# Kernel tuning notes

Measured on AMD Instinct MI355X. Metric: run time of the kernel, lower is better.

The kernel has to match this reference:

```python
import jax, jax.numpy as jnp
import numpy as np

K = 3        # deform kernel size
PAD = 1      # autopad(3)
STRIDE = 1

def _conv2d(x, w, b, stride, pad):
    out = jax.lax.conv_general_dilated(
        x, w, (stride, stride), [(pad, pad), (pad, pad)],
        dimension_numbers=('NCHW', 'OIHW', 'NCHW'))
    return out + b[None, :, None, None]

def setup_inputs() -> dict:
    key = jax.random.key(0)
    k1, k2, k3 = jax.random.split(key, 3)
    B, C1, C2, H, W = 16, 128, 128, 80, 80
    x = jax.random.normal(k1, (B, C1, H, W), dtype=jnp.float32)
    # offset-predicting conv: 2*K*K output channels, 3x3 kernel
    offset_w = jax.random.normal(k2, (2 * K * K, C1, 3, 3), dtype=jnp.float32) * 0.05
    offset_b = jnp.zeros((2 * K * K,), dtype=jnp.float32)
    fan_in = C1 * K * K
    weight = jax.random.normal(k3, (C2, C1, K, K), dtype=jnp.float32) * (1.0 / np.sqrt(fan_in))
    bias = jnp.zeros((C2,), dtype=jnp.float32)
    return {'x': x, 'offset_w': offset_w, 'offset_b': offset_b,
            'weight': weight, 'bias': bias}

def _deform_conv(x, offset, weight, bias):
    # x: [B,C,H,W]; offset: [B,2*K*K,Ho,Wo] in (dy,dx) pairs per kernel tap
    B, C, H, W = x.shape
    c2 = weight.shape[0]
    Ho, Wo = offset.shape[2], offset.shape[3]
    off = offset.reshape(B, K * K, 2, Ho, Wo)
    dy, dx = off[:, :, 0], off[:, :, 1]             # [B,KK,Ho,Wo]
    ii, jj = jnp.meshgrid(jnp.arange(K), jnp.arange(K), indexing='ij')
    ki = ii.reshape(-1).astype(jnp.float32)          # [KK]
    kj = jj.reshape(-1).astype(jnp.float32)
    hg = (jnp.arange(Ho) * STRIDE - PAD).astype(jnp.float32)
    wg = (jnp.arange(Wo) * STRIDE - PAD).astype(jnp.float32)
    py = hg[None, None, :, None] + ki[None, :, None, None] + dy  # [B,KK,Ho,Wo]
    px = wg[None, None, None, :] + kj[None, :, None, None] + dx
    y0 = jnp.floor(py); x0 = jnp.floor(px)
    wy1 = py - y0; wy0 = 1.0 - wy1
    wx1 = px - x0; wx0 = 1.0 - wx1

    def corner(yc, xc, wgt):
        valid = (yc >= 0) & (yc < H) & (xc >= 0) & (xc < W)
        yi = jnp.clip(yc, 0, H - 1).astype(jnp.int32)
        xi = jnp.clip(xc, 0, W - 1).astype(jnp.int32)
        # gather per batch: [B,C,KK,Ho,Wo]
        v = jax.vmap(lambda xb, yb, xb2: xb[:, yb, xb2])(x, yi, xi)
        return v * (wgt * valid.astype(x.dtype))[:, None]

    sampled = (corner(y0, x0, wy0 * wx0) + corner(y0, x0 + 1, wy0 * wx1)
               + corner(y0 + 1, x0, wy1 * wx0) + corner(y0 + 1, x0 + 1, wy1 * wx1))
    # grouped weighted sum (g=1): weight [c2, C, K, K] -> [c2, C, KK]
    out = jnp.einsum('bcphw,ocp->bohw', sampled, weight.reshape(c2, C, K * K))
    return out + bias[None, :, None, None]

def reference(x, offset_w, offset_b, weight, bias):
    offset = _conv2d(x, offset_w, offset_b, STRIDE, 1)  # [B, 2*K*K, Ho, Wo]
    return _deform_conv(x, offset, weight, bias)
```

## Files before the change

kernel.cpp:

```cpp
#include <hip/hip_runtime.h>

#define HH 80
#define WW 80
#define C1 128
#define C2 128
#define NB 16
#define HWSZ 6400
#define KKT 1152

typedef __attribute__((ext_vector_type(8))) short bf16x8;
typedef __attribute__((ext_vector_type(4))) float f32x4;

union PkU   { uint4 v; uint d[4]; bf16x8 h; };
union CornU { uint4 v; uint d[4]; };

__device__ inline ushort f2bf(float f) {
  unsigned u = __float_as_uint(f);
  return (ushort)((u + 0x7FFFu + ((u >> 16) & 1u)) >> 16);
}

__device__ inline uint cvtpk(float lo, float hi) {
  uint r;
  asm("v_cvt_pk_bf16_f32 %0, %1, %2" : "=v"(r) : "v"(lo), "v"(hi));
  return r;
}
__device__ inline float bfu_lo(uint w) { return __uint_as_float(w << 16); }
__device__ inline float bfu_hi(uint w) { return __uint_as_float(w & 0xFFFF0000u); }

__device__ inline void gload_lds16(const ushort* g, ushort* l) {
  __builtin_amdgcn_global_load_lds(
      (const __attribute__((address_space(1))) void*)g,
      (__attribute__((address_space(3))) void*)l, 16, 0, 0);
}

__global__ __launch_bounds__(256) void xpose_prep_kernel(
    const float* __restrict__ x, ushort* __restrict__ xt,
    const float* __restrict__ w, const float* __restrict__ ow,
    ushort* __restrict__ wbf, ushort* __restrict__ wobf,
    ushort* __restrict__ zpad) {
  __shared__ float ts[64][65];
  const int idx = blockIdx.x;
  const int tid = threadIdx.x;

  if (idx < 3200) {
    const int b = idx / 200;
    const int rem = idx % 200;
    const int c0 = (rem / 100) * 64;
    const int hw0 = (rem % 100) * 64;
    const int lane = tid & 63;

    #pragma unroll
    for (int it = 0; it < 16; it++) {
      int cl = (tid >> 6) + it * 4;
      ts[cl][lane] = x[((size_t)(b * C1 + c0 + cl)) * HWSZ + hw0 + lane];
    }
    __syncthreads();

    #pragma unroll
    for (int it = 0; it < 2; it++) {
      int u = tid + it * 256;
      int j = u >> 3, cg = u & 7;
      CornU pk;
      #pragma unroll
      for (int m = 0; m < 4; m++)
        pk.d[m] = cvtpk(ts[cg * 8 + 2 * m][j], ts[cg * 8 + 2 * m + 1][j]);
      *(uint4*)(xt + ((size_t)b * HWSZ + hw0 + j) * C1 + c0 + cg * 8) = pk.v;
    }
  } else {
    if (idx == 3200 && tid < 16) {
      uint4 z = {0u, 0u, 0u, 0u};
      ((uint4*)zpad)[tid] = z;
    }
    int o = (idx - 3200) * 256 + tid;
    if (o < C2 * KKT) {
      int j  = o & 7;
      int ch = (o >> 3) & 127;
      int kt = o >> 12;
      int kg = (o >> 10) & 3;
      int kprime = kt * 32 + kg * 8 + j;
      int p = kprime >> 7;
      int c = kprime & 127;
      wbf[o] = f2bf(w[(size_t)ch * KKT + c * 9 + p]);
    } else {
      int o2 = o - C2 * KKT;
      int j  = o2 & 7;
      int ch = (o2 >> 3) & 31;
      int kt = o2 >> 10;
      int kg = (o2 >> 8) & 3;
      int kprime = kt * 32 + kg * 8 + j;
      int p = kprime >> 7;
      int c = kprime & 127;
      wobf[o2] = (ch < 18) ? f2bf(ow[(size_t)ch * KKT + c * 9 + p]) : (ushort)0;
    }
  }
}

__global__ __launch_bounds__(256) void offset_mfma_kernel(
    const ushort* __restrict__ xt, const ushort* __restrict__ wobf,
    const ushort* __restrict__ zpad, const float* __restrict__ ob,
    float* __restrict__ offs) {
  const int bid = blockIdx.x;
  const int b = bid & 15;
  const int tile = bid >> 4;
  const int h0 = (tile / 5) * 4;
  const int w0 = (tile % 5) * 16;
  const int tid = threadIdx.x;
  const int lane = tid & 63;
  const int wave = tid >> 6;
  const int q = lane >> 4, c15 = lane & 15;

  __shared__ ushort w_obuf[4][1024];
  __shared__ ushort smp[4][16][128];

  const ushort* xtb = xt + (size_t)b * HWSZ * C1;
  f32x4 acc0 = {0.f, 0.f, 0.f, 0.f}, acc1 = {0.f, 0.f, 0.f, 0.f};

  #pragma unroll 1
  for (int p = 0; p < 9; ++p) {
    asm volatile("s_waitcnt lgkmcnt(0)" ::: "memory");
    __builtin_amdgcn_s_barrier();

    #pragma unroll
    for (int j = 0; j < 2; ++j)
      gload_lds16(wobf + (size_t)(4 * p + wave) * 1024 + (j * 64 + lane) * 8,
                  &w_obuf[wave][j * 512]);

    {
      const int row = h0 + wave + p / 3 - 1;
      #pragma unroll
      for (int jj = 0; jj < 4; ++jj) {
        const int pos = 4 * jj + q;
        const int col = w0 + pos + p % 3 - 1;
        const int sl = c15 ^ (pos & 7);
        const ushort* src =
            ((unsigned)row < (unsigned)HH && (unsigned)col < (unsigned)WW)
                ? xtb + ((size_t)row * WW + col) * C1 + sl * 8
                : zpad + sl * 8;
        gload_lds16(src, &smp[wave][4 * jj][0]);
      }
    }

    asm volatile("s_waitcnt vmcnt(0)" ::: "memory");
    __builtin_amdgcn_s_barrier();

    #pragma unroll
    for (int kk = 0; kk < 4; ++kk) {
      bf16x8 bfrag = *(const bf16x8*)
          &smp[wave][c15][(((4 * kk + q) ^ (c15 & 7)) * 8)];
      bf16x8 a0 = *(const bf16x8*)&w_obuf[kk][(q * 32 + c15) * 8];
      bf16x8 a1 = *(const bf16x8*)&w_obuf[kk][(q * 32 + 16 + c15) * 8];
      acc0 = __builtin_amdgcn_mfma_f32_16x16x32_bf16(a0, bfrag, acc0, 0, 0, 0);
      acc1 = __builtin_amdgcn_mfma_f32_16x16x32_bf16(a1, bfrag, acc1, 0, 0, 0);
    }
  }

  {
    const int ho = h0 + wave, wo = w0 + c15;
    #pragma unroll
    for (int r = 0; r < 4; r++) {
      int ch = q * 4 + r;
      if (ch < 18)
        offs[((size_t)b * 18 + ch) * HWSZ + ho * WW + wo] = acc0[r] + ob[ch];
      int ch1 = 16 + q * 4 + r;
      if (ch1 < 18)
        offs[((size_t)b * 18 + ch1) * HWSZ + ho * WW + wo] = acc1[r] + ob[ch1];
    }
  }
}

struct Geo { float f00, f01, f10, f11; int o00, o01, o10, o11; };

__device__ inline Geo make_geo(float4 cd) {
  Geo g;
  int y0 = (int)cd.x, x0 = (int)cd.y;
  float wy1 = cd.z, wx1 = cd.w;
  float fy0 = ((unsigned)y0 < (unsigned)HH) ? (1.f - wy1) : 0.f;
  float fy1 = ((unsigned)(y0 + 1) < (unsigned)HH) ? wy1 : 0.f;
  float fx0 = ((unsigned)x0 < (unsigned)WW) ? (1.f - wx1) : 0.f;
  float fx1 = ((unsigned)(x0 + 1) < (unsigned)WW) ? wx1 : 0.f;
  g.f00 = fy0 * fx0; g.f01 = fy0 * fx1;
  g.f10 = fy1 * fx0; g.f11 = fy1 * fx1;
  int r0 = min(max(y0, 0), HH - 1), r1 = min(max(y0 + 1, 0), HH - 1);
  int q0 = min(max(x0, 0), WW - 1), q1 = min(max(x0 + 1, 0), WW - 1);
  g.o00 = (r0 * WW + q0) * C1; g.o01 = (r0 * WW + q1) * C1;
  g.o10 = (r1 * WW + q0) * C1; g.o11 = (r1 * WW + q1) * C1;
  return g;
}

__global__ __launch_bounds__(256) void dconv_mfma_kernel(
    const ushort* __restrict__ xt, const float* __restrict__ offs,
    const ushort* __restrict__ wbf, const float* __restrict__ bias,
    float* __restrict__ out) {
  const int bid = blockIdx.x;
  const int b = bid & 15;
  const int tile = bid >> 4;
  const int h0 = (tile / 5) * 4;
  const int w0 = (tile % 5) * 16;
  const int tid = threadIdx.x;
  const int lane = tid & 63;
  const int wave = tid >> 6;
  const int q = lane >> 4, c15 = lane & 15;
  const int spos = wave * 16 + c15;

  __shared__ float4 crd[9][64];
  __shared__ ushort w_pbuf[4][4096];
  __shared__ ushort smp[4][16][128];

  const ushort* xtb = xt + (size_t)b * HWSZ * C1;

  {
    const int ho = h0 + wave, wo = w0 + c15;
    const float* obp = offs + (size_t)b * 18 * HWSZ + ho * WW + wo;
    #pragma unroll
    for (int p = 0; p < 9; ++p) {
      if ((p & 3) == q) {
        float dy = obp[(size_t)(2 * p) * HWSZ];
        float dx = obp[(size_t)(2 * p + 1) * HWSZ];
        float py = (float)(ho - 1 + p / 3) + dy;
        float px = (float)(wo - 1 + p % 3) + dx;
        float y0f = floorf(py), x0f = floorf(px);
        crd[p][spos] = make_float4(y0f, x0f, py - y0f, px - x0f);
      }
    }
  }

  const int jp = lane >> 4;
  const int s  = lane & 15;

  float4 fw[4];
  uint4  cr[4][4];

  auto issue_p = [&](int p) {
    #pragma unroll
    for (int jj = 0; jj < 4; ++jj) {
      Geo gg = make_geo(crd[p][wave * 16 + 4 * jj + jp]);
      fw[jj] = make_float4(gg.f00, gg.f01, gg.f10, gg.f11);
      const ushort* cp = xtb + s * 8;
      cr[jj][0] = *(const uint4*)(cp + gg.o00);
      cr[jj][1] = *(const uint4*)(cp + gg.o01);
      cr[jj][2] = *(const uint4*)(cp + gg.o10);
      cr[jj][3] = *(const uint4*)(cp + gg.o11);
    }
  };

  auto stage_p = [&](int p) {
    #pragma unroll
    for (int j = 0; j < 8; ++j)
      gload_lds16(wbf + ((size_t)(4 * p + wave)) * 4096 + (j * 64 + lane) * 8,
                  w_pbuf[wave] + j * 512);
  };

  auto bilinear_write = [&]() {
    #pragma unroll
    for (int jj = 0; jj < 4; ++jj) {
      const int pos = 4 * jj + jp;
      CornU u0, u1, u2, u3;
      PkU pk;
      u0.v = cr[jj][0]; u1.v = cr[jj][1]; u2.v = cr[jj][2]; u3.v = cr[jj][3];
      const float f00 = fw[jj].x, f01 = fw[jj].y, f10 = fw[jj].z, f11 = fw[jj].w;
      #pragma unroll
      for (int d = 0; d < 4; ++d) {
        float ol = f00 * bfu_lo(u0.d[d]);
        float oh = f00 * bfu_hi(u0.d[d]);
        ol = fmaf(f01, bfu_lo(u1.d[d]), ol);
        oh = fmaf(f01, bfu_hi(u1.d[d]), oh);
        ol = fmaf(f10, bfu_lo(u2.d[d]), ol);
        oh = fmaf(f10, bfu_hi(u2.d[d]), oh);
        ol = fmaf(f11, bfu_lo(u3.d[d]), ol);
        oh = fmaf(f11, bfu_hi(u3.d[d]), oh);
        pk.d[d] = cvtpk(ol, oh);
      }
      char* wp = (char*)&smp[wave][pos][0] + ((s * 16) ^ ((pos & 7) << 4));
      *(uint4*)wp = pk.v;
    }
  };

  f32x4 acc[8];
  #pragma unroll
  for (int mt = 0; mt < 8; mt++) acc[mt] = (f32x4){0.f, 0.f, 0.f, 0.f};

  issue_p(0);
  asm volatile("" ::: "memory");

  #pragma unroll 1
  for (int p = 0; p < 9; ++p) {
    asm volatile("s_waitcnt lgkmcnt(0)" ::: "memory");
    __builtin_amdgcn_s_barrier();

    stage_p(p);
    asm volatile("" ::: "memory");

    bilinear_write();

    if (p < 8) {
      issue_p(p + 1);
      asm volatile("" ::: "memory");
      asm volatile("s_waitcnt vmcnt(16)" ::: "memory");
    } else {
      asm volatile("s_waitcnt vmcnt(0)" ::: "memory");
    }
    __builtin_amdgcn_sched_barrier(0);
    asm volatile("s_waitcnt lgkmcnt(0)" ::: "memory");
    __builtin_amdgcn_s_barrier();

    #pragma unroll
    for (int kk = 0; kk < 4; ++kk) {
      const char* bp = (const char*)&smp[wave][c15][0] +
                       ((kk * 64 + q * 16) ^ ((c15 & 7) << 4));
      bf16x8 bfrag = *(const bf16x8*)bp;
      #pragma unroll
      for (int mt = 0; mt < 8; mt++) {
        bf16x8 afrag = *(const bf16x8*)&w_pbuf[kk][(q * 128 + mt * 16 + c15) * 8];
        acc[mt] = __builtin_amdgcn_mfma_f32_16x16x32_bf16(afrag, bfrag, acc[mt], 0, 0, 0);
      }
    }
  }

  {
    const int ho = h0 + wave, wo = w0 + c15;
    #pragma unroll
    for (int mt = 0; mt < 8; mt++) {
      #pragma unroll
      for (int r = 0; r < 4; r++) {
        int ch = mt * 16 + q * 4 + r;
        out[((size_t)b * C2 + ch) * HWSZ + ho * WW + wo] = acc[mt][r] + bias[ch];
      }
    }
  }
}

extern "C" void kernel_launch(void* const* d_in, const int* in_sizes, int n_in,
                              void* d_out, int out_size, void* d_ws, size_t ws_size,
                              hipStream_t stream) {
  const float* x    = (const float*)d_in[0];
  const float* ow   = (const float*)d_in[1];
  const float* ob   = (const float*)d_in[2];
  const float* wgt  = (const float*)d_in[3];
  const float* bias = (const float*)d_in[4];
  float* out = (float*)d_out;

  ushort* xt   = (ushort*)d_ws;
  float*  offs = (float*)((char*)d_ws + 26214400);
  ushort* wbf  = (ushort*)((char*)d_ws + 26214400 + 7372800);
  ushort* wobf = (ushort*)((char*)d_ws + 26214400 + 7372800 + 294912);
  ushort* zpad = (ushort*)((char*)d_ws + 26214400 + 7372800 + 294912 + 73728);

  xpose_prep_kernel<<<dim3(3920), dim3(256), 0, stream>>>(x, xt, wgt, ow, wbf, wobf, zpad);
  offset_mfma_kernel<<<dim3(1600), dim3(256), 0, stream>>>(xt, wobf, zpad, ob, offs);
  dconv_mfma_kernel<<<dim3(1600), dim3(256), 0, stream>>>(xt, offs, wbf, bias, out);
}
```

Baseline: 219.8 us.

## Fuse offset-predicting conv into deformable conv kernel via shared-memory offsets

Merges the offset MFMA conv kernel into the deformable conv kernel, so each block first computes its tile's 18 offset channels into shared memory and then reads them directly. This removes one kernel launch and the global write and read of the offset tensor. The offset weight buffer is aliased onto the deform weight buffer in LDS. The cost is extra LDS and longer per-block work before the main loop.

Measured after the change: 216.1 us. Within noise of the previous version (-1.7%).

```diff
diff --git a/kernel.cpp b/kernel.cpp
--- a/kernel.cpp
+++ b/kernel.cpp
@@ -95,79 +95,6 @@
   }
 }
 
-__global__ __launch_bounds__(256) void offset_mfma_kernel(
-    const ushort* __restrict__ xt, const ushort* __restrict__ wobf,
-    const ushort* __restrict__ zpad, const float* __restrict__ ob,
-    float* __restrict__ offs) {
-  const int bid = blockIdx.x;
-  const int b = bid & 15;
-  const int tile = bid >> 4;
-  const int h0 = (tile / 5) * 4;
-  const int w0 = (tile % 5) * 16;
-  const int tid = threadIdx.x;
-  const int lane = tid & 63;
-  const int wave = tid >> 6;
-  const int q = lane >> 4, c15 = lane & 15;
-
-  __shared__ ushort w_obuf[4][1024];
-  __shared__ ushort smp[4][16][128];
-
-  const ushort* xtb = xt + (size_t)b * HWSZ * C1;
-  f32x4 acc0 = {0.f, 0.f, 0.f, 0.f}, acc1 = {0.f, 0.f, 0.f, 0.f};
-
-  #pragma unroll 1
-  for (int p = 0; p < 9; ++p) {
-    asm volatile("s_waitcnt lgkmcnt(0)" ::: "memory");
-    __builtin_amdgcn_s_barrier();
-
-    #pragma unroll
-    for (int j = 0; j < 2; ++j)
-      gload_lds16(wobf + (size_t)(4 * p + wave) * 1024 + (j * 64 + lane) * 8,
-                  &w_obuf[wave][j * 512]);
-
-    {
-      const int row = h0 + wave + p / 3 - 1;
-      #pragma unroll
-      for (int jj = 0; jj < 4; ++jj) {
-        const int pos = 4 * jj + q;
-        const int col = w0 + pos + p % 3 - 1;
-        const int sl = c15 ^ (pos & 7);
-        const ushort* src =
-            ((unsigned)row < (unsigned)HH && (unsigned)col < (unsigned)WW)
-                ? xtb + ((size_t)row * WW + col) * C1 + sl * 8
-                : zpad + sl * 8;
-        gload_lds16(src, &smp[wave][4 * jj][0]);
-      }
-    }
-
-    asm volatile("s_waitcnt vmcnt(0)" ::: "memory");
-    __builtin_amdgcn_s_barrier();
-
-    #pragma unroll
-    for (int kk = 0; kk < 4; ++kk) {
-      bf16x8 bfrag = *(const bf16x8*)
-          &smp[wave][c15][(((4 * kk + q) ^ (c15 & 7)) * 8)];
-      bf16x8 a0 = *(const bf16x8*)&w_obuf[kk][(q * 32 + c15) * 8];
-      bf16x8 a1 = *(const bf16x8*)&w_obuf[kk][(q * 32 + 16 + c15) * 8];
-      acc0 = __builtin_amdgcn_mfma_f32_16x16x32_bf16(a0, bfrag, acc0, 0, 0, 0);
-      acc1 = __builtin_amdgcn_mfma_f32_16x16x32_bf16(a1, bfrag, acc1, 0, 0, 0);
-    }
-  }
-
-  {
-    const int ho = h0 + wave, wo = w0 + c15;
-    #pragma unroll
-    for (int r = 0; r < 4; r++) {
-      int ch = q * 4 + r;
-      if (ch < 18)
-        offs[((size_t)b * 18 + ch) * HWSZ + ho * WW + wo] = acc0[r] + ob[ch];
-      int ch1 = 16 + q * 4 + r;
-      if (ch1 < 18)
-        offs[((size_t)b * 18 + ch1) * HWSZ + ho * WW + wo] = acc1[r] + ob[ch1];
-    }
-  }
-}
-
 struct Geo { float f00, f01, f10, f11; int o00, o01, o10, o11; };
 
 __device__ inline Geo make_geo(float4 cd) {
@@ -187,8 +114,9 @@
   return g;
 }
 
-__global__ __launch_bounds__(256) void dconv_mfma_kernel(
-    const ushort* __restrict__ xt, const float* __restrict__ offs,
+__global__ __launch_bounds__(256) void dconv_fused_kernel(
+    const ushort* __restrict__ xt, const ushort* __restrict__ wobf,
+    const ushort* __restrict__ zpad, const float* __restrict__ ob,
     const ushort* __restrict__ wbf, const float* __restrict__ bias,
     float* __restrict__ out) {
   const int bid = blockIdx.x;
@@ -205,17 +133,72 @@
   __shared__ float4 crd[9][64];
   __shared__ ushort w_pbuf[4][4096];
   __shared__ ushort smp[4][16][128];
+  __shared__ float  obuf[18][64];
+
+  ushort (*w_obuf)[1024] = reinterpret_cast<ushort (*)[1024]>(&w_pbuf[0][0]);
 
   const ushort* xtb = xt + (size_t)b * HWSZ * C1;
+
+  {
+    f32x4 acc0 = {0.f, 0.f, 0.f, 0.f}, acc1 = {0.f, 0.f, 0.f, 0.f};
+
+    #pragma unroll 1
+    for (int p = 0; p < 9; ++p) {
+      asm volatile("s_waitcnt lgkmcnt(0)" ::: "memory");
+      __builtin_amdgcn_s_barrier();
+
+      #pragma unroll
+      for (int j = 0; j < 2; ++j)
+        gload_lds16(wobf + (size_t)(4 * p + wave) * 1024 + (j * 64 + lane) * 8,
+                    &w_obuf[wave][j * 512]);
+
+      {
+        const int row = h0 + wave + p / 3 - 1;
+        #pragma unroll
+        for (int jj = 0; jj < 4; ++jj) {
+          const int pos = 4 * jj + q;
+          const int col = w0 + pos + p % 3 - 1;
+          const int sl = c15 ^ (pos & 7);
+          const ushort* src =
+              ((unsigned)row < (unsigned)HH && (unsigned)col < (unsigned)WW)
+                  ? xtb + ((size_t)row * WW + col) * C1 + sl * 8
+                  : zpad + sl * 8;
+          gload_lds16(src, &smp[wave][4 * jj][0]);
+        }
+      }
+
+      asm volatile("s_waitcnt vmcnt(0)" ::: "memory");
+      __builtin_amdgcn_s_barrier();
+
+      #pragma unroll
+      for (int kk = 0; kk < 4; ++kk) {
+        bf16x8 bfrag = *(const bf16x8*)
+            &smp[wave][c15][(((4 * kk + q) ^ (c15 & 7)) * 8)];
+        bf16x8 a0 = *(const bf16x8*)&w_obuf[kk][(q * 32 + c15) * 8];
+        bf16x8 a1 = *(const bf16x8*)&w_obuf[kk][(q * 32 + 16 + c15) * 8];
+        acc0 = __builtin_amdgcn_mfma_f32_16x16x32_bf16(a0, bfrag, acc0, 0, 0, 0);
+        acc1 = __builtin_amdgcn_mfma_f32_16x16x32_bf16(a1, bfrag, acc1, 0, 0, 0);
+      }
+    }
+
+    #pragma unroll
+    for (int r = 0; r < 4; r++) {
+      int ch = q * 4 + r;
+      obuf[ch][spos] = acc0[r] + ob[ch];
+    }
+    if (q == 0) {
+      obuf[16][spos] = acc1[0] + ob[16];
+      obuf[17][spos] = acc1[1] + ob[17];
+    }
+  }
 
   {
     const int ho = h0 + wave, wo = w0 + c15;
-    const float* obp = offs + (size_t)b * 18 * HWSZ + ho * WW + wo;
     #pragma unroll
     for (int p = 0; p < 9; ++p) {
       if ((p & 3) == q) {
-        float dy = obp[(size_t)(2 * p) * HWSZ];
-        float dx = obp[(size_t)(2 * p + 1) * HWSZ];
+        float dy = obuf[2 * p][spos];
+        float dx = obuf[2 * p + 1][spos];
         float py = (float)(ho - 1 + p / 3) + dy;
         float px = (float)(wo - 1 + p % 3) + dx;
         float y0f = floorf(py), x0f = floorf(px);
@@ -340,12 +323,10 @@
   float* out = (float*)d_out;
 
   ushort* xt   = (ushort*)d_ws;
-  float*  offs = (float*)((char*)d_ws + 26214400);
-  ushort* wbf  = (ushort*)((char*)d_ws + 26214400 + 7372800);
-  ushort* wobf = (ushort*)((char*)d_ws + 26214400 + 7372800 + 294912);
-  ushort* zpad = (ushort*)((char*)d_ws + 26214400 + 7372800 + 294912 + 73728);
+  ushort* wbf  = (ushort*)((char*)d_ws + 26214400);
+  ushort* wobf = (ushort*)((char*)d_ws + 26214400 + 294912);
+  ushort* zpad = (ushort*)((char*)d_ws + 26214400 + 294912 + 73728);
 
   xpose_prep_kernel<<<dim3(3920), dim3(256), 0, stream>>>(x, xt, wgt, ow, wbf, wobf, zpad);
-  offset_mfma_kernel<<<dim3(1600), dim3(256), 0, stream>>>(xt, wobf, zpad, ob, offs);
-  dconv_mfma_kernel<<<dim3(1600), dim3(256), 0, stream>>>(xt, offs, wbf, bias, out);
-}
+  dconv_fused_kernel<<<dim3(1600), dim3(256), 0, stream>>>(xt, wobf, zpad, ob, wbf, bias, out);
+}
```
